# Kernel optimization log

Hardware: AMD Instinct MI355X
Metric: run time of the kernel (lower is better)

## Reference

```python
import jax, jax.numpy as jnp
import numpy as np

OUT_F, IN_F = 8192, 8192
RATIO = 0.05


def setup_inputs() -> dict:
    rng = np.random.default_rng(0)
    # Simulate the quantization performed in OrthoLinear.__init__ with numpy.
    w = (rng.standard_normal((OUT_F, IN_F)) * 0.02).astype(np.float32)
    w_abs = np.abs(w)
    k_idx = min(int(IN_F * 0.995), IN_F - 1)
    # torch.kthvalue(k) = k-th smallest (1-indexed) -> partition index k-1
    robust_max = np.partition(w_abs, k_idx - 1, axis=1)[:, k_idx - 1][:, None]
    robust_max = np.maximum(robust_max, 1e-6)
    scales = (robust_max / 7.0).astype(np.float32)
    w_int = np.clip(np.round(w / scales), -7, 7).astype(np.float32)
    resid = w - w_int * scales
    # top-k |residual| entries form the sparse CSR correction
    k = max(int(resid.size * RATIO), 1)
    metric = np.abs(resid).ravel()
    idx = np.argpartition(metric, -k)[-k:]
    idx.sort()
    rows = idx // IN_F
    cols = (idx % IN_F).astype(np.int32)
    vals = resid.ravel()[idx].astype(np.float16)
    ptr = np.zeros(OUT_F + 1, np.int32)
    ptr[1:] = np.cumsum(np.bincount(rows, minlength=OUT_F)).astype(np.int32)
    # pack two int4 (offset by +8) per byte: even cols -> low nibble, odd -> high
    offs = (w_int + 8.0).astype(np.uint8)
    packed = (offs[:, 0::2] | (offs[:, 1::2] << 4)).astype(np.int32)
    x = jax.random.normal(jax.random.key(0), (4, 8, IN_F), jnp.float32)
    return {
        "x": x,
        "base_packed": jnp.asarray(packed),
        "scales": jnp.asarray(scales.reshape(-1)),
        "ortho_vals": jnp.asarray(vals),
        "ortho_indices": jnp.asarray(cols),
        "ortho_ptr": jnp.asarray(ptr),
        "alpha": jnp.float32(1.0),
    }


def reference(x, base_packed, scales, ortho_vals, ortho_indices, ortho_ptr, alpha):
    lead = x.shape[:-1]
    in_f = x.shape[-1]
    out_f = base_packed.shape[0]
    xf = x.reshape(-1, in_f).astype(jnp.float32)  # [N, in]
    # dequantize packed int4 base weight: interleave low/high nibbles
    low = base_packed & 0xF
    high = (base_packed >> 4) & 0xF
    w_int = jnp.stack([low, high], axis=-1).reshape(out_f, in_f).astype(jnp.float32) - 8.0
    w_base = w_int * scales[:, None]  # [out, in]
    # CSR residual -> scatter into dense [out, in] (disjoint coords), then GEMM
    nnz = ortho_vals.shape[0]
    row_ids = jnp.searchsorted(ortho_ptr, jnp.arange(nnz, dtype=jnp.int32), side="right") - 1
    w_res = jnp.zeros((out_f, in_f), jnp.float32).at[row_ids, ortho_indices].add(
        ortho_vals.astype(jnp.float32)
    )
    out = xf @ w_base.T + alpha * (xf @ w_res.T)  # [N, out]
    return out.reshape(lead + (out_f,))
```

## Files before the change

kernel.cpp:

```cpp
#include <hip/hip_runtime.h>


#define IN_F 8192
#define OUT_F 8192
#define NROW 32
#define KSPLIT 8
#define KSEG (IN_F / KSPLIT)
#define KS 64
#define NSTEP (KSEG / KS)
#define PK_TILE 8192
#define X_TILE 4096
#define BUF_SZ (PK_TILE + 2 * X_TILE)
#define SLICE (NROW * OUT_F)

typedef __attribute__((ext_vector_type(8))) short short8v;
typedef __attribute__((ext_vector_type(4))) float f32x4;

union Frag {
  int4 v;
  unsigned int u[4];
  short8v s;
};

__device__ __forceinline__ unsigned int cvt_pk_bf16(float lo, float hi) {
  unsigned int r;
  asm("v_cvt_pk_bf16_f32 %0, %1, %2" : "=v"(r) : "v"(lo), "v"(hi));
  return r;
}

__device__ __forceinline__ unsigned short f2bf(float f) {
  unsigned int u = __float_as_uint(f);
  u += 0x7FFFu + ((u >> 16) & 1u);
  return (unsigned short)(u >> 16);
}

__global__ __launch_bounds__(256) void prep_kernel(
    const float* __restrict__ x, unsigned short* __restrict__ x_hi,
    unsigned short* __restrict__ x_lo, unsigned short* __restrict__ xTb) {
  __shared__ unsigned short T[64 * 33];
  int tid = threadIdx.x;
  int k0 = blockIdx.x * 64;
  int kk = tid & 63;
  int ng = tid >> 6;
#pragma unroll
  for (int p = 0; p < 8; ++p) {
    int n = p * 4 + ng;
    int idx = n * IN_F + k0 + kk;
    float v = x[idx];
    unsigned short h = f2bf(v);
    float hf = __uint_as_float((unsigned int)h << 16);
    unsigned short l = f2bf(v - hf);
    x_hi[idx] = h;
    x_lo[idx] = l;
    T[kk * 33 + n] = h;
  }
  __syncthreads();
  int kr = tid >> 2, q = tid & 3;
  unsigned int s0 = T[kr * 33 + q * 8 + 0], s1 = T[kr * 33 + q * 8 + 1];
  unsigned int s2 = T[kr * 33 + q * 8 + 2], s3 = T[kr * 33 + q * 8 + 3];
  unsigned int s4 = T[kr * 33 + q * 8 + 4], s5 = T[kr * 33 + q * 8 + 5];
  unsigned int s6 = T[kr * 33 + q * 8 + 6], s7 = T[kr * 33 + q * 8 + 7];
  int4 wv;
  wv.x = (int)(s0 | (s1 << 16));
  wv.y = (int)(s2 | (s3 << 16));
  wv.z = (int)(s4 | (s5 << 16));
  wv.w = (int)(s6 | (s7 << 16));
  ((int4*)xTb)[(size_t)(k0 + kr) * 4 + q] = wv;
}

__global__ __launch_bounds__(256) void dense_kernel(
    const int* __restrict__ packed, const float* __restrict__ scales,
    const unsigned short* __restrict__ x_hi,
    const unsigned short* __restrict__ x_lo, float* __restrict__ part) {
  __shared__ char lds[2][BUF_SZ];
  int tid = threadIdx.x;
  int lane = tid & 63;
  int w = tid >> 6;
  int og = blockIdx.x >> 3;
  int g = blockIdx.x & 7;
  int lo16 = lane & 15;
  int lhi = lane >> 4;

  int L0 = tid * 16;
  int pr0 = L0 >> 7;
  int pb0 = (L0 & 127) ^ ((pr0 & 7) << 4);
  const char* pkB = (const char*)packed;
  const char* psrc0 = pkB + (size_t)(og * 64 + pr0) * 16384 + g * 2048 + pb0;
  const char* psrc1 = pkB + (size_t)(og * 64 + pr0 + 32) * 16384 + g * 2048 + pb0;
  int xr = tid >> 3;
  int xb = ((tid & 7) * 16) ^ ((xr & 7) << 4);
  const char* xhsrc = (const char*)x_hi + (size_t)xr * (IN_F * 2) + g * 2048 + xb;
  const char* xlsrc = (const char*)x_lo + (size_t)xr * (IN_F * 2) + g * 2048 + xb;
  int woff = w * 1024;

#define STAGE(s, b)                                                          \
  {                                                                          \
    int so_ = (s) * 128;                                                     \
    __builtin_amdgcn_global_load_lds((const unsigned int*)(psrc0 + so_),     \
        (unsigned int*)(&lds[b][0] + woff), 16, 0, 0);                       \
    __builtin_amdgcn_global_load_lds((const unsigned int*)(psrc1 + so_),     \
        (unsigned int*)(&lds[b][4096] + woff), 16, 0, 0);                    \
    __builtin_amdgcn_global_load_lds((const unsigned int*)(xhsrc + so_),     \
        (unsigned int*)(&lds[b][PK_TILE] + woff), 16, 0, 0);                 \
    __builtin_amdgcn_global_load_lds((const unsigned int*)(xlsrc + so_),     \
        (unsigned int*)(&lds[b][PK_TILE + X_TILE] + woff), 16, 0, 0);        \
  }

  f32x4 acc0 = {0.f, 0.f, 0.f, 0.f};
  f32x4 acc1 = {0.f, 0.f, 0.f, 0.f};
  int prow = w * 16 + lo16;
  int pswz = (prow & 7) << 4;
  int xswz = (lo16 & 7) << 4;

#define COMPCHUNK(b, cp)                                                      \
  {                                                                           \
    int pby = (cp) * 64 + 16 * lhi;                                           \
    Frag bb, a0h, a0l, a1h, a1l;                                              \
    bb.v = *(const int4*)&lds[b][prow * 128 + (pby ^ pswz)];                  \
    a0h.v = *(const int4*)&lds[b][PK_TILE + lo16 * 128 + (pby ^ xswz)];       \
    a0l.v = *(const int4*)&lds[b][PK_TILE + X_TILE + lo16 * 128 + (pby ^ xswz)]; \
    a1h.v = *(const int4*)&lds[b][PK_TILE + (lo16 + 16) * 128 + (pby ^ xswz)];   \
    a1l.v = *(const int4*)&lds[b][PK_TILE + X_TILE + (lo16 + 16) * 128 + (pby ^ xswz)]; \
    Frag bf;                                                                  \
    bf.u[0] = cvt_pk_bf16((float)(bb.v.x & 15) - 8.0f, (float)(bb.v.x >> 4) - 8.0f); \
    bf.u[1] = cvt_pk_bf16((float)(bb.v.y & 15) - 8.0f, (float)(bb.v.y >> 4) - 8.0f); \
    bf.u[2] = cvt_pk_bf16((float)(bb.v.z & 15) - 8.0f, (float)(bb.v.z >> 4) - 8.0f); \
    bf.u[3] = cvt_pk_bf16((float)(bb.v.w & 15) - 8.0f, (float)(bb.v.w >> 4) - 8.0f); \
    acc0 = __builtin_amdgcn_mfma_f32_16x16x32_bf16(a0h.s, bf.s, acc0, 0, 0, 0); \
    acc0 = __builtin_amdgcn_mfma_f32_16x16x32_bf16(a0l.s, bf.s, acc0, 0, 0, 0); \
    acc1 = __builtin_amdgcn_mfma_f32_16x16x32_bf16(a1h.s, bf.s, acc1, 0, 0, 0); \
    acc1 = __builtin_amdgcn_mfma_f32_16x16x32_bf16(a1l.s, bf.s, acc1, 0, 0, 0); \
  }

  STAGE(0, 0)
  for (int s = 0; s < NSTEP; ++s) {
    int b = s & 1;
    if (s + 1 < NSTEP) {
      STAGE(s + 1, (s + 1) & 1)
      asm volatile("s_waitcnt vmcnt(4)" ::: "memory");
    } else {
      asm volatile("s_waitcnt vmcnt(0)" ::: "memory");
    }
    __syncthreads();
    COMPCHUNK(b, 0)
    COMPCHUNK(b, 1)
    __syncthreads();
  }
#undef STAGE
#undef COMPCHUNK

  int o = og * 64 + w * 16 + lo16;
  float sc = scales[o];
  float* ps = part + (size_t)g * SLICE;
#pragma unroll
  for (int r = 0; r < 4; ++r) {
    int m = lhi * 4 + r;
    ps[(size_t)m * OUT_F + o] = sc * acc0[r];
    ps[(size_t)(m + 16) * OUT_F + o] = sc * acc1[r];
  }
}

__global__ __launch_bounds__(256) void sparse_kernel(
    const float* __restrict__ vals, const int* __restrict__ cols,
    const int* __restrict__ rptr, const float* __restrict__ alphap,
    const unsigned short* __restrict__ xTb, float* __restrict__ part8) {
  __shared__ float red[4][64 * 33];
  int tid = threadIdx.x;
  int lane = tid & 63;
  int w = tid >> 6;
  float alpha = alphap[0];
  float* R = red[w];
#pragma unroll 1
  for (int rr = 0; rr < 2; ++rr) {
    int ro = blockIdx.x * 8 + w * 2 + rr;
    int js = rptr[ro], je = rptr[ro + 1];
    float acc[32];
#pragma unroll
    for (int i = 0; i < 32; ++i) acc[i] = 0.f;

    int j = js + lane;
    float vc = 0.f;
    int cc = 0;
    if (j < je) { vc = vals[j]; cc = cols[j]; }
    while (j < je) {
      int jn = j + 64;
      float vn = 0.f;
      int cn = 0;
      if (jn < je) { vn = vals[jn]; cn = cols[jn]; }
      const int4* xp = (const int4*)(xTb + (size_t)cc * NROW);
      int4 q0 = xp[0], q1 = xp[1], q2 = xp[2], q3 = xp[3];
#define UNP(dw, base)                                                          \
  {                                                                            \
    unsigned int ud = (unsigned int)(dw);                                      \
    acc[base] = fmaf(vc, __uint_as_float(ud << 16), acc[base]);                \
    acc[base + 1] = fmaf(vc, __uint_as_float(ud & 0xFFFF0000u), acc[base + 1]); \
  }
      UNP(q0.x, 0) UNP(q0.y, 2) UNP(q0.z, 4) UNP(q0.w, 6)
      UNP(q1.x, 8) UNP(q1.y, 10) UNP(q1.z, 12) UNP(q1.w, 14)
      UNP(q2.x, 16) UNP(q2.y, 18) UNP(q2.z, 20) UNP(q2.w, 22)
      UNP(q3.x, 24) UNP(q3.y, 26) UNP(q3.z, 28) UNP(q3.w, 30)
#undef UNP
      j = jn;
      vc = vn;
      cc = cn;
    }
#pragma unroll
    for (int i = 0; i < 32; ++i) R[lane * 33 + i] = acc[i];
    int cidx = lane & 31;
    int h = lane >> 5;
    float sum = 0.f;
#pragma unroll
    for (int r2 = 0; r2 < 32; ++r2) sum += R[(h * 32 + r2) * 33 + cidx];
    sum += __shfl_xor(sum, 32, 64);
    if (lane < 32) part8[(size_t)lane * OUT_F + ro] = alpha * sum;
  }
}

__global__ __launch_bounds__(256) void reduce_kernel(
    const float* __restrict__ part, float* __restrict__ out) {
  int i = blockIdx.x * 256 + threadIdx.x;
  const float4* p4 = (const float4*)part;
  float4 s = p4[i];
#pragma unroll
  for (int sl = 1; sl < 9; ++sl) {
    float4 t = p4[i + sl * (SLICE / 4)];
    s.x += t.x; s.y += t.y; s.z += t.z; s.w += t.w;
  }
  ((float4*)out)[i] = s;
}

extern "C" void kernel_launch(void* const* d_in, const int* in_sizes, int n_in,
                              void* d_out, int out_size, void* d_ws, size_t ws_size,
                              hipStream_t stream) {
  const float* x = (const float*)d_in[0];
  const int* packed = (const int*)d_in[1];
  const float* scales = (const float*)d_in[2];
  const float* vals = (const float*)d_in[3];
  const int* cols = (const int*)d_in[4];
  const int* rptr = (const int*)d_in[5];
  const float* alphap = (const float*)d_in[6];
  float* out = (float*)d_out;

  unsigned short* x_hi = (unsigned short*)d_ws;
  unsigned short* x_lo = x_hi + NROW * IN_F;
  unsigned short* xTb = x_lo + NROW * IN_F;
  float* part = (float*)(xTb + NROW * IN_F);

  prep_kernel<<<IN_F / 64, 256, 0, stream>>>(x, x_hi, x_lo, xTb);
  dense_kernel<<<(OUT_F / 64) * KSPLIT, 256, 0, stream>>>(
      packed, scales, x_hi, x_lo, part);
  sparse_kernel<<<OUT_F / 8, 256, 0, stream>>>(
      vals, cols, rptr, alphap, xTb, part + (size_t)8 * SLICE);
  reduce_kernel<<<(SLICE / 4) / 256, 256, 0, stream>>>(part, out);
}
```

Measured before the change: 263.8 us.

## Drop bf16 low-part split of x and fuse partial reduction into sparse kernel

Removes the hi/lo bf16 split of the activations, so the dense MFMA loop loads one x tile per stage and issues half as many MFMAs, and the prep kernel no longer writes x_lo. The separate reduce kernel is also removed: the sparse kernel now sums the eight dense K-split partials directly and writes the output, saving one launch and one full pass over the partial buffers. The cost is precision, since x is now rounded to plain bf16 and the dense GEMM loses the compensation term. That could push errors past tolerance for an 8192-long dot product.

```diff
diff --git a/kernel.cpp b/kernel.cpp
--- a/kernel.cpp
+++ b/kernel.cpp
@@ -10,7 +10,7 @@
 #define NSTEP (KSEG / KS)
 #define PK_TILE 8192
 #define X_TILE 4096
-#define BUF_SZ (PK_TILE + 2 * X_TILE)
+#define BUF_SZ (PK_TILE + X_TILE)
 #define SLICE (NROW * OUT_F)
 
 typedef __attribute__((ext_vector_type(8))) short short8v;
@@ -36,7 +36,7 @@
 
 __global__ __launch_bounds__(256) void prep_kernel(
     const float* __restrict__ x, unsigned short* __restrict__ x_hi,
-    unsigned short* __restrict__ x_lo, unsigned short* __restrict__ xTb) {
+    unsigned short* __restrict__ xTb) {
   __shared__ unsigned short T[64 * 33];
   int tid = threadIdx.x;
   int k0 = blockIdx.x * 64;
@@ -46,12 +46,8 @@
   for (int p = 0; p < 8; ++p) {
     int n = p * 4 + ng;
     int idx = n * IN_F + k0 + kk;
-    float v = x[idx];
-    unsigned short h = f2bf(v);
-    float hf = __uint_as_float((unsigned int)h << 16);
-    unsigned short l = f2bf(v - hf);
+    unsigned short h = f2bf(x[idx]);
     x_hi[idx] = h;
-    x_lo[idx] = l;
     T[kk * 33 + n] = h;
   }
   __syncthreads();
@@ -70,8 +66,7 @@
 
 __global__ __launch_bounds__(256) void dense_kernel(
     const int* __restrict__ packed, const float* __restrict__ scales,
-    const unsigned short* __restrict__ x_hi,
-    const unsigned short* __restrict__ x_lo, float* __restrict__ part) {
+    const unsigned short* __restrict__ x_hi, float* __restrict__ part) {
   __shared__ char lds[2][BUF_SZ];
   int tid = threadIdx.x;
   int lane = tid & 63;
@@ -90,7 +85,6 @@
   int xr = tid >> 3;
   int xb = ((tid & 7) * 16) ^ ((xr & 7) << 4);
   const char* xhsrc = (const char*)x_hi + (size_t)xr * (IN_F * 2) + g * 2048 + xb;
-  const char* xlsrc = (const char*)x_lo + (size_t)xr * (IN_F * 2) + g * 2048 + xb;
   int woff = w * 1024;
 
 #define STAGE(s, b)                                                          \
@@ -102,8 +96,6 @@
         (unsigned int*)(&lds[b][4096] + woff), 16, 0, 0);                    \
     __builtin_amdgcn_global_load_lds((const unsigned int*)(xhsrc + so_),     \
         (unsigned int*)(&lds[b][PK_TILE] + woff), 16, 0, 0);                 \
-    __builtin_amdgcn_global_load_lds((const unsigned int*)(xlsrc + so_),     \
-        (unsigned int*)(&lds[b][PK_TILE + X_TILE] + woff), 16, 0, 0);        \
   }
 
   f32x4 acc0 = {0.f, 0.f, 0.f, 0.f};
@@ -115,21 +107,17 @@
 #define COMPCHUNK(b, cp)                                                      \
   {                                                                           \
     int pby = (cp) * 64 + 16 * lhi;                                           \
-    Frag bb, a0h, a0l, a1h, a1l;                                              \
+    Frag bb, a0h, a1h;                                                        \
     bb.v = *(const int4*)&lds[b][prow * 128 + (pby ^ pswz)];                  \
     a0h.v = *(const int4*)&lds[b][PK_TILE + lo16 * 128 + (pby ^ xswz)];       \
-    a0l.v = *(const int4*)&lds[b][PK_TILE + X_TILE + lo16 * 128 + (pby ^ xswz)]; \
-    a1h.v = *(const int4*)&lds[b][PK_TILE + (lo16 + 16) * 128 + (pby ^ xswz)];   \
-    a1l.v = *(const int4*)&lds[b][PK_TILE + X_TILE + (lo16 + 16) * 128 + (pby ^ xswz)]; \
+    a1h.v = *(const int4*)&lds[b][PK_TILE + (lo16 + 16) * 128 + (pby ^ xswz)]; \
     Frag bf;                                                                  \
     bf.u[0] = cvt_pk_bf16((float)(bb.v.x & 15) - 8.0f, (float)(bb.v.x >> 4) - 8.0f); \
     bf.u[1] = cvt_pk_bf16((float)(bb.v.y & 15) - 8.0f, (float)(bb.v.y >> 4) - 8.0f); \
     bf.u[2] = cvt_pk_bf16((float)(bb.v.z & 15) - 8.0f, (float)(bb.v.z >> 4) - 8.0f); \
     bf.u[3] = cvt_pk_bf16((float)(bb.v.w & 15) - 8.0f, (float)(bb.v.w >> 4) - 8.0f); \
     acc0 = __builtin_amdgcn_mfma_f32_16x16x32_bf16(a0h.s, bf.s, acc0, 0, 0, 0); \
-    acc0 = __builtin_amdgcn_mfma_f32_16x16x32_bf16(a0l.s, bf.s, acc0, 0, 0, 0); \
     acc1 = __builtin_amdgcn_mfma_f32_16x16x32_bf16(a1h.s, bf.s, acc1, 0, 0, 0); \
-    acc1 = __builtin_amdgcn_mfma_f32_16x16x32_bf16(a1l.s, bf.s, acc1, 0, 0, 0); \
   }
 
   STAGE(0, 0)
@@ -137,7 +125,7 @@
     int b = s & 1;
     if (s + 1 < NSTEP) {
       STAGE(s + 1, (s + 1) & 1)
-      asm volatile("s_waitcnt vmcnt(4)" ::: "memory");
+      asm volatile("s_waitcnt vmcnt(3)" ::: "memory");
     } else {
       asm volatile("s_waitcnt vmcnt(0)" ::: "memory");
     }
@@ -163,7 +151,8 @@
 __global__ __launch_bounds__(256) void sparse_kernel(
     const float* __restrict__ vals, const int* __restrict__ cols,
     const int* __restrict__ rptr, const float* __restrict__ alphap,
-    const unsigned short* __restrict__ xTb, float* __restrict__ part8) {
+    const unsigned short* __restrict__ xTb, const float* __restrict__ part,
+    float* __restrict__ out) {
   __shared__ float red[4][64 * 33];
   int tid = threadIdx.x;
   int lane = tid & 63;
@@ -212,21 +201,14 @@
 #pragma unroll
     for (int r2 = 0; r2 < 32; ++r2) sum += R[(h * 32 + r2) * 33 + cidx];
     sum += __shfl_xor(sum, 32, 64);
-    if (lane < 32) part8[(size_t)lane * OUT_F + ro] = alpha * sum;
-  }
-}
-
-__global__ __launch_bounds__(256) void reduce_kernel(
-    const float* __restrict__ part, float* __restrict__ out) {
-  int i = blockIdx.x * 256 + threadIdx.x;
-  const float4* p4 = (const float4*)part;
-  float4 s = p4[i];
-#pragma unroll
-  for (int sl = 1; sl < 9; ++sl) {
-    float4 t = p4[i + sl * (SLICE / 4)];
-    s.x += t.x; s.y += t.y; s.z += t.z; s.w += t.w;
-  }
-  ((float4*)out)[i] = s;
+    if (lane < 32) {
+      float t = alpha * sum;
+      const float* pp = part + (size_t)lane * OUT_F + ro;
+#pragma unroll
+      for (int g2 = 0; g2 < 8; ++g2) t += pp[(size_t)g2 * SLICE];
+      out[(size_t)lane * OUT_F + ro] = t;
+    }
+  }
 }
 
 extern "C" void kernel_launch(void* const* d_in, const int* in_sizes, int n_in,
@@ -242,14 +224,12 @@
   float* out = (float*)d_out;
 
   unsigned short* x_hi = (unsigned short*)d_ws;
-  unsigned short* x_lo = x_hi + NROW * IN_F;
-  unsigned short* xTb = x_lo + NROW * IN_F;
+  unsigned short* xTb = x_hi + NROW * IN_F;
   float* part = (float*)(xTb + NROW * IN_F);
 
-  prep_kernel<<<IN_F / 64, 256, 0, stream>>>(x, x_hi, x_lo, xTb);
+  prep_kernel<<<IN_F / 64, 256, 0, stream>>>(x, x_hi, xTb);
   dense_kernel<<<(OUT_F / 64) * KSPLIT, 256, 0, stream>>>(
-      packed, scales, x_hi, x_lo, part);
+      packed, scales, x_hi, part);
   sparse_kernel<<<OUT_F / 8, 256, 0, stream>>>(
-      vals, cols, rptr, alphap, xTb, part + (size_t)8 * SLICE);
-  reduce_kernel<<<(SLICE / 4) / 256, 256, 0, stream>>>(part, out);
-}
+      vals, cols, rptr, alphap, xTb, part, out);
+}
```

After: 275.2 us. +4.3%, slower.
